# Optimization experiments

Hardware: AMD Instinct MI355X
Metric: run time of the kernel (lower is better)

Reference implementation:

```python
import jax, jax.numpy as jnp
import numpy as np

N_DST = [50000, 10000, 2048]
HEADS = 4


def setup_inputs() -> dict:
    key = jax.random.key(0)
    ks = jax.random.split(key, 32)
    d = {}
    d["x"] = jax.random.normal(ks[0], (200000, 128), jnp.float32)
    # conv fc weights [in, H*D], attn vectors [H, D], bias [H*D]; skip [in, out]+bias
    conv_dims = [(128, 64), (256, 64), (256, 47)]   # (in, per-head out D)
    skip_dims = [(128, 256), (256, 256), (256, 47)]
    for l, ((cin, dph), (sin, sout)) in enumerate(zip(conv_dims, skip_dims)):
        d[f"W{l}"] = 0.1 * jax.random.normal(ks[1 + 5 * l], (cin, HEADS * dph), jnp.float32)
        d[f"al{l}"] = 0.1 * jax.random.normal(ks[2 + 5 * l], (HEADS, dph), jnp.float32)
        d[f"ar{l}"] = 0.1 * jax.random.normal(ks[3 + 5 * l], (HEADS, dph), jnp.float32)
        d[f"b{l}"] = jnp.zeros((HEADS * dph,), jnp.float32)
        d[f"Ws{l}"] = 0.1 * jax.random.normal(ks[4 + 5 * l], (sin, sout), jnp.float32)
        d[f"bs{l}"] = jnp.zeros((sout,), jnp.float32)
    edge_cfg = [(800000, 200000, 50000), (400000, 50000, 10000), (100000, 10000, 2048)]
    for l, (ne, ns, nd) in enumerate(edge_cfg):
        d[f"src{l}"] = jax.random.randint(ks[20 + 2 * l], (ne,), 0, ns, jnp.int32)
        d[f"dst{l}"] = jax.random.randint(ks[21 + 2 * l], (ne,), 0, nd, jnp.int32)
    return d


def gat_conv(h_src, h_dst, src, dst, n_dst, W, al, ar, b):
    H, D = al.shape
    fs = (h_src @ W).reshape(-1, H, D)   # [n_src, H, D]
    fd = (h_dst @ W).reshape(-1, H, D)   # [n_dst, H, D]
    el = jnp.einsum("nhd,hd->nh", fs, al)
    er = jnp.einsum("nhd,hd->nh", fd, ar)
    e = jax.nn.leaky_relu(el[src] + er[dst], 0.2)          # [E, H]
    emax = jax.ops.segment_max(e, dst, num_segments=n_dst)  # stable softmax
    ee = jnp.exp(e - emax[dst])
    denom = jax.ops.segment_sum(ee, dst, num_segments=n_dst)
    alpha = ee / denom[dst]
    msg = fs[src] * alpha[:, :, None]                      # [E, H, D]
    rst = jax.ops.segment_sum(msg, dst, num_segments=n_dst)
    return rst + b.reshape(1, H, D)


def reference(x, W0, al0, ar0, b0, Ws0, bs0, W1, al1, ar1, b1, Ws1, bs1,
              W2, al2, ar2, b2, Ws2, bs2, src0, dst0, src1, dst1, src2, dst2):
    h = x
    # layer 0
    h_res = h[:N_DST[0]]
    h = gat_conv(h, h_res, src0, dst0, N_DST[0], W0, al0, ar0, b0).reshape(N_DST[0], -1)
    h = jax.nn.elu(h + h_res @ Ws0 + bs0)
    # layer 1
    h_res = h[:N_DST[1]]
    h = gat_conv(h, h_res, src1, dst1, N_DST[1], W1, al1, ar1, b1).reshape(N_DST[1], -1)
    h = jax.nn.elu(h + h_res @ Ws1 + bs1)
    # layer 2: mean over heads, no activation
    h_res = h[:N_DST[2]]
    h = gat_conv(h, h_res, src2, dst2, N_DST[2], W2, al2, ar2, b2).mean(axis=1)
    h = h + h_res @ Ws2 + bs2
    return jax.nn.log_softmax(h, axis=-1)
```

## Files before the change

### kernel.cpp

```cpp
#include <hip/hip_runtime.h>
#include <hip/hip_bf16.h>
#include <cmath>

#define HEADS 4
typedef __hip_bfloat16 bf16;
typedef short short8 __attribute__((ext_vector_type(8)));
typedef unsigned short us8 __attribute__((ext_vector_type(8)));
typedef float floatx4 __attribute__((ext_vector_type(4)));
typedef float floatx2 __attribute__((ext_vector_type(2)));
typedef unsigned int u32;

__device__ inline float bf2f(unsigned short u) {
    union { unsigned u; float f; } c; c.u = ((unsigned)u) << 16; return c.f;
}
__device__ inline short f2bs(float f) {
    bf16 h = __float2bfloat16(f);
    return *reinterpret_cast<short*>(&h);
}
__device__ __forceinline__ unsigned pack_bf16(float a, float b) {
    return (((unsigned)(unsigned short)f2bs(b)) << 16) | (unsigned short)f2bs(a);
}
__device__ __forceinline__ unsigned pack_fp8x4(float a, float b, float c, float d) {
    unsigned lo = __builtin_amdgcn_cvt_pk_fp8_f32(a, b, 0, false);
    return __builtin_amdgcn_cvt_pk_fp8_f32(c, d, lo, true);
}

__device__ __forceinline__ void ld_lds16(const void* g, void* l) {
    __builtin_amdgcn_global_load_lds((const __attribute__((address_space(1))) u32*)g,
                                     (__attribute__((address_space(3))) u32*)l, 16, 0, 0);
}

__device__ const int g_ND[3]   = {50000, 10000, 2048};
__device__ const int g_OOFF[3] = {0, 50001, 60002};
__device__ const int g_NE[3]   = {800000, 400000, 100000};
__device__ const int g_SOFF[3] = {0, 800000, 1200000};
__device__ const int g_S[3]    = {391, 79, 16};

#define NBIN 128
#define NBLK 128
#define MAXB 8192
#define MAXS 391
#define PF 4

__global__ void precast_all(const float* __restrict__ W0, const float* __restrict__ W1,
                            const float* __restrict__ W2, const float* __restrict__ W3,
                            const float* __restrict__ W4,
                            bf16* __restrict__ B0, bf16* __restrict__ B1, bf16* __restrict__ B2,
                            bf16* __restrict__ B3, bf16* __restrict__ B4)
{
    int y = blockIdx.y;
    const int Ks[5] = {128, 256, 256, 128, 256};
    const int Ns[5] = {256, 256, 188, 256, 256};
    const float* W = (y == 0) ? W0 : (y == 1) ? W1 : (y == 2) ? W2 : (y == 3) ? W3 : W4;
    bf16* B = (y == 0) ? B0 : (y == 1) ? B1 : (y == 2) ? B2 : (y == 3) ? B3 : B4;
    int K = Ks[y], N = Ns[y], sz = K * N;
    for (int i = blockIdx.x * blockDim.x + threadIdx.x; i < sz; i += gridDim.x * blockDim.x) {
        int n = i / K, k = i % K;
        B[i] = __float2bfloat16(W[(size_t)k * N + n]);
    }
}

template<int FUSE, int EL, int OUT8, int AF32>
__global__ __launch_bounds__(512)
void gemm_mfma(const void* __restrict__ Ain, const bf16* __restrict__ Bt,
               const bf16* __restrict__ add, const float* __restrict__ bias,
               const float* __restrict__ al, const float* __restrict__ ar,
               float* __restrict__ el, float* __restrict__ er,
               void* __restrict__ Cb, int M, int N, int K, int nd)
{
    const int BK = 64;
    __shared__ short As[128 * BK];
    __shared__ short Bs[256 * BK];
    int tid = threadIdx.x;
    int wave = tid >> 6, lane = tid & 63;
    int q = lane >> 4, r = lane & 15;
    int row0 = blockIdx.y * 128;
    int wm = (wave >> 2) * 64, wn = (wave & 3) * 64;

    const short* B16 = (const short*)Bt;
    int srow = tid >> 3;
    int scol = ((tid & 7) ^ (srow & 7)) * 8;
    const short* ga0; const short* ga1;
    const float* gaf0; const float* gaf1;
    if (AF32) {
        int arow0 = min(row0 + srow, M - 1);
        int arow1 = min(row0 + 64 + srow, M - 1);
        gaf0 = (const float*)Ain + (size_t)arow0 * K + scol;
        gaf1 = (const float*)Ain + (size_t)arow1 * K + scol;
        ga0 = ga1 = nullptr;
    } else {
        const short* A16 = (const short*)Ain;
        ga0 = A16 + (size_t)(row0 + srow) * K + scol;
        ga1 = ga0 + (size_t)64 * K;
        gaf0 = gaf1 = nullptr;
    }
    const short* gb = B16 + (size_t)srow * K + scol;
    char* la = (char*)As + tid * 16;
    char* lb = (char*)Bs + tid * 16;

    floatx4 zero = {0.f, 0.f, 0.f, 0.f};
    floatx4 acc[4][4];
#pragma unroll
    for (int i = 0; i < 4; i++)
#pragma unroll
        for (int j = 0; j < 4; j++) acc[i][j] = zero;

    for (int k0 = 0; k0 < K; k0 += BK) {
        ld_lds16(gb,                   lb);
        ld_lds16(gb + (size_t)64 * K,  lb + 8192);
        ld_lds16(gb + (size_t)128 * K, lb + 16384);
        ld_lds16(gb + (size_t)192 * K, lb + 24576);
        gb += BK;
        if (AF32) {
            float4 a0 = *(const float4*)gaf0;
            float4 a1 = *(const float4*)(gaf0 + 4);
            float4 b0 = *(const float4*)gaf1;
            float4 b1 = *(const float4*)(gaf1 + 4);
            uint4 w0 = {pack_bf16(a0.x, a0.y), pack_bf16(a0.z, a0.w),
                        pack_bf16(a1.x, a1.y), pack_bf16(a1.z, a1.w)};
            uint4 w1 = {pack_bf16(b0.x, b0.y), pack_bf16(b0.z, b0.w),
                        pack_bf16(b1.x, b1.y), pack_bf16(b1.z, b1.w)};
            *(uint4*)la = w0;
            *(uint4*)(la + 8192) = w1;
            gaf0 += BK; gaf1 += BK;
        } else {
            ld_lds16(ga0, la);
            ld_lds16(ga1, la + 8192);
            ga0 += BK; ga1 += BK;
        }
        __syncthreads();
#pragma unroll
        for (int ks = 0; ks < 2; ks++) {
            int gr = (((ks << 2) | q) ^ (r & 7)) * 8;
            short8 af[4], bfr[4];
#pragma unroll
            for (int mt = 0; mt < 4; mt++)
                af[mt] = *(short8*)&As[(wm + mt * 16 + r) * BK + gr];
#pragma unroll
            for (int nt = 0; nt < 4; nt++)
                bfr[nt] = *(short8*)&Bs[(wn + nt * 16 + r) * BK + gr];
#pragma unroll
            for (int mt = 0; mt < 4; mt++)
#pragma unroll
                for (int nt = 0; nt < 4; nt++)
                    acc[mt][nt] = __builtin_amdgcn_mfma_f32_16x16x32_bf16(bfr[nt], af[mt], acc[mt][nt], 0, 0, 0);
        }
        __syncthreads();
    }

#pragma unroll
    for (int mt = 0; mt < 4; mt++) {
        int grow = row0 + wm + mt * 16 + r;
        if (grow >= M) continue;
#pragma unroll
        for (int nt = 0; nt < 4; nt++) {
            int n0 = wn + nt * 16 + q * 4;
            floatx4 v = acc[mt][nt];
            if (FUSE == 1) {
                ushort4 ad = *(const ushort4*)&add[(size_t)grow * N + n0];
                float4 bi = *(const float4*)&bias[n0];
                v[0] += bf2f(ad.x) + bi.x;
                v[1] += bf2f(ad.y) + bi.y;
                v[2] += bf2f(ad.z) + bi.z;
                v[3] += bf2f(ad.w) + bi.w;
#pragma unroll
                for (int e = 0; e < 4; e++) v[e] = (v[e] > 0.f) ? v[e] : (__expf(v[e]) - 1.f);
            }
            if (OUT8) {
                *(u32*)((unsigned char*)Cb + (size_t)grow * N + n0) =
                    pack_fp8x4(v[0], v[1], v[2], v[3]);
            } else if (n0 + 3 < N) {
                uint2 o = {pack_bf16(v[0], v[1]), pack_bf16(v[2], v[3])};
                *(uint2*)((unsigned short*)Cb + (size_t)grow * N + n0) = o;
            } else {
#pragma unroll
                for (int e = 0; e < 4; e++)
                    if (n0 + e < N)
                        ((unsigned short*)Cb)[(size_t)grow * N + n0 + e] = (unsigned short)f2bs(v[e]);
            }
        }
    }

    if (EL) {
        int head = wave & 3;
#pragma unroll
        for (int mt = 0; mt < 4; mt++) {
            float pl = 0.f, pr = 0.f;
#pragma unroll
            for (int nt = 0; nt < 4; nt++) {
                int nn = nt * 16 + q * 4;
                float4 av = *(const float4*)&al[head * 64 + nn];
                float4 rv = *(const float4*)&ar[head * 64 + nn];
                floatx4 v = acc[mt][nt];
                pl += v[0] * av.x + v[1] * av.y + v[2] * av.z + v[3] * av.w;
                pr += v[0] * rv.x + v[1] * rv.y + v[2] * rv.z + v[3] * rv.w;
            }
            pl += __shfl_xor(pl, 16); pl += __shfl_xor(pl, 32);
            pr += __shfl_xor(pr, 16); pr += __shfl_xor(pr, 32);
            int grow = row0 + wm + mt * 16 + r;
            if (lane < 16 && grow < M) {
                el[grow * 4 + head] = pl;
                if (grow < nd) er[grow * 4 + head] = pr;
            }
        }
    }
}

__global__ void el_er_kernel(const bf16* __restrict__ fs, const float* __restrict__ al,
                             const float* __restrict__ ar, float* __restrict__ el,
                             float* __restrict__ er, int nd, int D)
{
    int n = blockIdx.x;
    int h = threadIdx.x >> 6;
    int d = threadIdx.x & 63;
    int HD = HEADS * D;
    float v = 0.f, a = 0.f, rr = 0.f;
    if (d < D) {
        v = __bfloat162float(fs[(size_t)n * HD + h * D + d]);
        a = al[h * D + d];
        rr = ar[h * D + d];
    }
    float pl = v * a, pr = v * rr;
    for (int off = 32; off; off >>= 1) {
        pl += __shfl_down(pl, off);
        pr += __shfl_down(pr, off);
    }
    if (d == 0) {
        el[n * HEADS + h] = pl;
        if (n < nd) er[n * HEADS + h] = pr;
    }
}

__global__ __launch_bounds__(256)
void bin_hist(const int* __restrict__ d0, const int* __restrict__ d1,
              const int* __restrict__ d2, int* __restrict__ blockhist)
{
    int l = blockIdx.y;
    const int* dst = (l == 0) ? d0 : (l == 1) ? d1 : d2;
    int ne = g_NE[l], S = g_S[l];
    __shared__ int h[NBIN];
    for (int i = threadIdx.x; i < NBIN; i += blockDim.x) h[i] = 0;
    __syncthreads();
    int per = (ne + NBLK - 1) / NBLK;
    int st = blockIdx.x * per;
    int en = min(st + per, ne);
    for (int i = st + threadIdx.x; i < en; i += blockDim.x)
        atomicAdd(&h[dst[i] / S], 1);
    __syncthreads();
    for (int i = threadIdx.x; i < NBIN; i += blockDim.x)
        blockhist[(l * NBIN + i) * NBLK + blockIdx.x] = h[i];
}

__global__ void coarse_scan(const int* __restrict__ blockhist, int* __restrict__ bbase,
                            int* __restrict__ offs)
{
    int l = blockIdx.x;
    int t = threadIdx.x;
    __shared__ int s[NBIN];
    int tot = 0;
    for (int k = 0; k < NBLK; k++) tot += blockhist[(l * NBIN + t) * NBLK + k];
    s[t] = tot;
    __syncthreads();
    for (int off = 1; off < NBIN; off <<= 1) {
        int a = (t >= off) ? s[t - off] : 0;
        __syncthreads();
        s[t] += a;
        __syncthreads();
    }
    bbase[l * (NBIN + 1) + t + 1] = s[t];
    if (t == 0) {
        bbase[l * (NBIN + 1)] = 0;
        offs[g_OOFF[l] + g_ND[l]] = g_NE[l];
    }
}

__global__ void bin_scan(const int* __restrict__ blockhist, const int* __restrict__ bbase,
                         int* __restrict__ base)
{
    int l = blockIdx.y, bin = blockIdx.x;
    int t = threadIdx.x;
    __shared__ int s[NBLK];
    int v = blockhist[(l * NBIN + bin) * NBLK + t];
    s[t] = v;
    __syncthreads();
    for (int off = 1; off < NBLK; off <<= 1) {
        int a = (t >= off) ? s[t - off] : 0;
        __syncthreads();
        s[t] += a;
        __syncthreads();
    }
    base[(l * NBIN + bin) * NBLK + t] = bbase[l * (NBIN + 1) + bin] + s[t] - v;
}

__global__ __launch_bounds__(256)
void bin_scatter(const int* __restrict__ s0, const int* __restrict__ d0,
                 const int* __restrict__ s1, const int* __restrict__ d1,
                 const int* __restrict__ s2, const int* __restrict__ d2,
                 const int* __restrict__ base, int* __restrict__ stage)
{
    int l = blockIdx.y;
    const int* src = (l == 0) ? s0 : (l == 1) ? s1 : s2;
    const int* dst = (l == 0) ? d0 : (l == 1) ? d1 : d2;
    int ne = g_NE[l], S = g_S[l], soff = g_SOFF[l];
    __shared__ int cur[NBIN];
    for (int i = threadIdx.x; i < NBIN; i += blockDim.x)
        cur[i] = base[(l * NBIN + i) * NBLK + blockIdx.x];
    __syncthreads();
    int per = (ne + NBLK - 1) / NBLK;
    int st = blockIdx.x * per;
    int en = min(st + per, ne);
    for (int i = st + threadIdx.x; i < en; i += blockDim.x) {
        int dv = dst[i];
        int b = dv / S;
        int ldst = dv - b * S;
        int p = atomicAdd(&cur[b], 1);
        stage[soff + p] = src[i] | (ldst << 18);
    }
}

__global__ __launch_bounds__(256)
void bin_expand(const int* __restrict__ stage, const int* __restrict__ bbase,
                int* __restrict__ offs, int* __restrict__ ssrc)
{
    int l = blockIdx.y, b = blockIdx.x;
    int S = g_S[l], nd = g_ND[l], ooff = g_OOFF[l], soff = g_SOFF[l];
    int dlo = b * S;
    if (dlo >= nd) return;
    int dhi = min(dlo + S, nd);
    int base = bbase[l * (NBIN + 1) + b];
    int end  = bbase[l * (NBIN + 1) + b + 1];
    int cnt  = end - base;
    int tid = threadIdx.x;
    __shared__ int sdata[MAXB];
    __shared__ int outb[MAXB];
    __shared__ int lh[512];
    __shared__ int lcur[MAXS];
    lh[tid] = 0; lh[tid + 256] = 0;
    __syncthreads();
    if (cnt <= MAXB) {
        for (int i = tid; i < cnt; i += 256) {
            int v = stage[soff + base + i];
            sdata[i] = v;
            atomicAdd(&lh[v >> 18], 1);
        }
        __syncthreads();
        for (int off = 1; off < 512; off <<= 1) {
            int a0 = (tid >= off) ? lh[tid - off] : 0;
            int a1 = lh[tid + 256 - off];
            __syncthreads();
            lh[tid] += a0; lh[tid + 256] += a1;
            __syncthreads();
        }
        for (int d = tid; d < dhi - dlo; d += 256) {
            int ex = (d == 0) ? 0 : lh[d - 1];
            offs[ooff + dlo + d] = base + ex;
            lcur[d] = ex;
        }
        __syncthreads();
        for (int i = tid; i < cnt; i += 256) {
            int v = sdata[i];
            int p = atomicAdd(&lcur[v >> 18], 1);
            outb[p] = v & 0x3FFFF;
        }
        __syncthreads();
        for (int i = tid; i < cnt; i += 256)
            ssrc[soff + base + i] = outb[i];
    } else {
        for (int i = tid; i < cnt; i += 256)
            atomicAdd(&lh[stage[soff + base + i] >> 18], 1);
        __syncthreads();
        for (int off = 1; off < 512; off <<= 1) {
            int a0 = (tid >= off) ? lh[tid - off] : 0;
            int a1 = lh[tid + 256 - off];
            __syncthreads();
            lh[tid] += a0; lh[tid + 256] += a1;
            __syncthreads();
        }
        for (int d = tid; d < dhi - dlo; d += 256) {
            int ex = (d == 0) ? 0 : lh[d - 1];
            offs[ooff + dlo + d] = base + ex;
            lcur[d] = ex;
        }
        __syncthreads();
        for (int i = tid; i < cnt; i += 256) {
            int v = stage[soff + base + i];
            int p = atomicAdd(&lcur[v >> 18], 1);
            ssrc[soff + base + p] = v & 0x3FFFF;
        }
    }
}

__global__ __launch_bounds__(256)
void attn_agg64(const unsigned char* __restrict__ fs8, const float* __restrict__ el,
                const float* __restrict__ er, const float* __restrict__ b,
                const int* __restrict__ offs, const int* __restrict__ ssrc,
                bf16* __restrict__ rst, int nd)
{
    int wave = threadIdx.x >> 6, lane = threadIdx.x & 63;
    int n = blockIdx.x * 4 + wave;
    if (n >= nd) return;
    int s0 = offs[n], s1 = offs[n + 1];
    float4 erv = *(const float4*)&er[(size_t)n * 4];
    int half = lane >> 5, sub = lane & 31, head = sub >> 3;
    float eh = (head == 0) ? erv.x : (head == 1) ? erv.y : (head == 2) ? erv.z : erv.w;

    floatx2 acc[4];
#pragma unroll
    for (int j = 0; j < 4; j++) acc[j] = (floatx2){0.f, 0.f};
    float s = 0.f;

    int cnt = s1 - s0;
    int npairs = cnt >> 1;
    int i = s0 + half;
    if (npairs > 0) {
        int sid = ssrc[i];
        float ev = el[(size_t)sid * 4 + head];
        uint2 f = *(const uint2*)&fs8[(size_t)sid * 256 + sub * 8];
        for (int p = 1; p < npairs; p++) {
            i += 2;
            int sid2 = ssrc[i];
            float ev2 = el[(size_t)sid2 * 4 + head];
            uint2 f2 = *(const uint2*)&fs8[(size_t)sid2 * 256 + sub * 8];
            float e = ev + eh; e = (e > 0.f) ? e : 0.2f * e;
            float a = __expf(fminf(e, 60.f));
            s += a;
            floatx2 aa = {a, a};
            acc[0] = __builtin_elementwise_fma((floatx2)__builtin_amdgcn_cvt_pk_f32_fp8(f.x, false), aa, acc[0]);
            acc[1] = __builtin_elementwise_fma((floatx2)__builtin_amdgcn_cvt_pk_f32_fp8(f.x, true),  aa, acc[1]);
            acc[2] = __builtin_elementwise_fma((floatx2)__builtin_amdgcn_cvt_pk_f32_fp8(f.y, false), aa, acc[2]);
            acc[3] = __builtin_elementwise_fma((floatx2)__builtin_amdgcn_cvt_pk_f32_fp8(f.y, true),  aa, acc[3]);
            ev = ev2; f = f2;
        }
        float e = ev + eh; e = (e > 0.f) ? e : 0.2f * e;
        float a = __expf(fminf(e, 60.f));
        s += a;
        floatx2 aa = {a, a};
        acc[0] = __builtin_elementwise_fma((floatx2)__builtin_amdgcn_cvt_pk_f32_fp8(f.x, false), aa, acc[0]);
        acc[1] = __builtin_elementwise_fma((floatx2)__builtin_amdgcn_cvt_pk_f32_fp8(f.x, true),  aa, acc[1]);
        acc[2] = __builtin_elementwise_fma((floatx2)__builtin_amdgcn_cvt_pk_f32_fp8(f.y, false), aa, acc[2]);
        acc[3] = __builtin_elementwise_fma((floatx2)__builtin_amdgcn_cvt_pk_f32_fp8(f.y, true),  aa, acc[3]);
    }
    if (cnt & 1) {
        int idx = s1 - 1;
        int sid = ssrc[idx];
        float ev = el[(size_t)sid * 4 + head];
        uint2 f = *(const uint2*)&fs8[(size_t)sid * 256 + sub * 8];
        float e = ev + eh; e = (e > 0.f) ? e : 0.2f * e;
        float a = __expf(fminf(e, 60.f));
        if (half) a = 0.f;
        s += a;
        floatx2 aa = {a, a};
        acc[0] = __builtin_elementwise_fma((floatx2)__builtin_amdgcn_cvt_pk_f32_fp8(f.x, false), aa, acc[0]);
        acc[1] = __builtin_elementwise_fma((floatx2)__builtin_amdgcn_cvt_pk_f32_fp8(f.x, true),  aa, acc[1]);
        acc[2] = __builtin_elementwise_fma((floatx2)__builtin_amdgcn_cvt_pk_f32_fp8(f.y, false), aa, acc[2]);
        acc[3] = __builtin_elementwise_fma((floatx2)__builtin_amdgcn_cvt_pk_f32_fp8(f.y, true),  aa, acc[3]);
    }
    s += __shfl_xor(s, 32);
#pragma unroll
    for (int j = 0; j < 4; j++) {
        acc[j].x += __shfl_xor(acc[j].x, 32);
        acc[j].y += __shfl_xor(acc[j].y, 32);
    }
    if (half == 0) {
        float inv = (s > 0.f) ? 1.f / s : 0.f;
        float4 b0 = *(const float4*)&b[sub * 8];
        float4 b1 = *(const float4*)&b[sub * 8 + 4];
        us8 o;
        o[0] = (unsigned short)f2bs(acc[0].x * inv + b0.x);
        o[1] = (unsigned short)f2bs(acc[0].y * inv + b0.y);
        o[2] = (unsigned short)f2bs(acc[1].x * inv + b0.z);
        o[3] = (unsigned short)f2bs(acc[1].y * inv + b0.w);
        o[4] = (unsigned short)f2bs(acc[2].x * inv + b1.x);
        o[5] = (unsigned short)f2bs(acc[2].y * inv + b1.y);
        o[6] = (unsigned short)f2bs(acc[3].x * inv + b1.z);
        o[7] = (unsigned short)f2bs(acc[3].y * inv + b1.w);
        *(us8*)&((unsigned short*)rst)[(size_t)n * 256 + sub * 8] = o;
    }
}

__global__ __launch_bounds__(256)
void attn_final_gen(const bf16* __restrict__ fs, const float* __restrict__ el,
                    const float* __restrict__ er, const float* __restrict__ b,
                    const int* __restrict__ offs, const int* __restrict__ ssrc,
                    const bf16* __restrict__ h2, const float* __restrict__ Ws,
                    const float* __restrict__ bs, float* __restrict__ out,
                    int D, int nd)
{
    __shared__ int slds[4][64];
    __shared__ __align__(16) float alds[4][64][4];
    __shared__ float flds[4][192];
    __shared__ unsigned short hlds[4][256];
    int wave = threadIdx.x >> 6, lane = threadIdx.x & 63;
    int n = blockIdx.x * 4 + wave;
    int HD = HEADS * D;
    int s0 = offs[n], s1 = offs[n + 1];
    int cnt = s1 - s0;
    float4 erv = *(const float4*)&er[(size_t)n * 4];
    const unsigned short* fsu = (const unsigned short*)fs;
    const unsigned short* h2u = (const unsigned short*)h2;

    *(ushort4*)&hlds[wave][lane * 4] = *(const ushort4*)&h2u[(size_t)n * 256 + lane * 4];

    bool act = (4 * lane) < HD;
    int h_[4];
#pragma unroll
    for (int j = 0; j < 4; j++) {
        int e = 4 * lane + j;
        h_[j] = (e < HD) ? (e / D) : 0;
    }
    float acc[4] = {0.f, 0.f, 0.f, 0.f};
    float sp0 = 0.f, sp1 = 0.f, sp2 = 0.f, sp3 = 0.f;

    for (int c0 = 0; c0 < cnt; c0 += 64) {
        int nc = min(cnt - c0, 64);
        if (lane < nc) {
            int sid = ssrc[s0 + c0 + lane];
            float4 ev = *(const float4*)&el[(size_t)sid * 4];
            float e0 = ev.x + erv.x; e0 = (e0 > 0.f) ? e0 : 0.2f * e0;
            float e1 = ev.y + erv.y; e1 = (e1 > 0.f) ? e1 : 0.2f * e1;
            float e2 = ev.z + erv.z; e2 = (e2 > 0.f) ? e2 : 0.2f * e2;
            float e3 = ev.w + erv.w; e3 = (e3 > 0.f) ? e3 : 0.2f * e3;
            float a0 = __expf(fminf(e0, 60.f));
            float a1 = __expf(fminf(e1, 60.f));
            float a2 = __expf(fminf(e2, 60.f));
            float a3 = __expf(fminf(e3, 60.f));
            sp0 += a0; sp1 += a1; sp2 += a2; sp3 += a3;
            slds[wave][lane] = sid;
            alds[wave][lane][0] = a0;
            alds[wave][lane][1] = a1;
            alds[wave][lane][2] = a2;
            alds[wave][lane][3] = a3;
        }
        __builtin_amdgcn_wave_barrier();
        float4 aq[PF]; ushort4 fq[PF];
#pragma unroll
        for (int k = 0; k < PF; k++) {
            if (k < nc) {
                int sid = slds[wave][k];
                aq[k] = *(const float4*)&alds[wave][k][0];
                fq[k] = act ? *(const ushort4*)&fsu[(size_t)sid * HD + 4 * lane]
                            : ushort4{0, 0, 0, 0};
            }
        }
        for (int eb = 0; eb < nc; eb += PF) {
#pragma unroll
            for (int k = 0; k < PF; k++) {
                int e = eb + k;
                if (e >= nc) break;
                float4 a4 = aq[k];
                ushort4 f = fq[k];
                int en = e + PF;
                if (en < nc) {
                    int sid = slds[wave][en];
                    aq[k] = *(const float4*)&alds[wave][en][0];
                    fq[k] = act ? *(const ushort4*)&fsu[(size_t)sid * HD + 4 * lane]
                                : ushort4{0, 0, 0, 0};
                }
                unsigned short fa[4] = {f.x, f.y, f.z, f.w};
#pragma unroll
                for (int j = 0; j < 4; j++) {
                    int hj = h_[j];
                    float av = (hj == 0) ? a4.x : (hj == 1) ? a4.y : (hj == 2) ? a4.z : a4.w;
                    acc[j] += av * bf2f(fa[j]);
                }
            }
        }
        __builtin_amdgcn_wave_barrier();
    }

#pragma unroll
    for (int off = 32; off; off >>= 1) {
        sp0 += __shfl_xor(sp0, off);
        sp1 += __shfl_xor(sp1, off);
        sp2 += __shfl_xor(sp2, off);
        sp3 += __shfl_xor(sp3, off);
    }
    if (act) {
#pragma unroll
        for (int j = 0; j < 4; j++) {
            int e4 = 4 * lane + j;
            int hj = h_[j];
            float sv = (hj == 0) ? sp0 : (hj == 1) ? sp1 : (hj == 2) ? sp2 : sp3;
            float o = (sv > 0.f) ? acc[j] / sv : 0.f;
            flds[wave][e4] = o + b[e4];
        }
    }
    __builtin_amdgcn_wave_barrier();

    const int C = 47;
    int c = lane;
    float v = -INFINITY;
    if (c < C) {
        float mean = 0.25f * (flds[wave][c] + flds[wave][C + c] +
                              flds[wave][2 * C + c] + flds[wave][3 * C + c]);
        float dot = 0.f;
#pragma unroll 4
        for (int k = 0; k < 256; k++)
            dot += bf2f(hlds[wave][k]) * Ws[k * C + c];
        v = mean + dot + bs[c];
    }
    float mx = v;
#pragma unroll
    for (int off = 32; off; off >>= 1) mx = fmaxf(mx, __shfl_xor(mx, off));
    float ex = (c < C) ? __expf(v - mx) : 0.f;
    float sum = ex;
#pragma unroll
    for (int off = 32; off; off >>= 1) sum += __shfl_xor(sum, off);
    if (c < C) out[n * C + c] = v - mx - logf(sum);
}

extern "C" void kernel_launch(void* const* d_in, const int* in_sizes, int n_in,
                              void* d_out, int out_size, void* d_ws, size_t ws_size,
                              hipStream_t stream)
{
    const float* x = (const float*)d_in[0];
    const float* W[3]  = {(const float*)d_in[1],  (const float*)d_in[7],  (const float*)d_in[13]};
    const float* al[3] = {(const float*)d_in[2],  (const float*)d_in[8],  (const float*)d_in[14]};
    const float* ar[3] = {(const float*)d_in[3],  (const float*)d_in[9],  (const float*)d_in[15]};
    const float* bb[3] = {(const float*)d_in[4],  (const float*)d_in[10], (const float*)d_in[16]};
    const float* Ws[3] = {(const float*)d_in[5],  (const float*)d_in[11], (const float*)d_in[17]};
    const float* bs[3] = {(const float*)d_in[6],  (const float*)d_in[12], (const float*)d_in[18]};
    const int* srcp[3] = {(const int*)d_in[19], (const int*)d_in[21], (const int*)d_in[23]};
    const int* dstp[3] = {(const int*)d_in[20], (const int*)d_in[22], (const int*)d_in[24]};

    char* p = (char*)d_ws;
    auto alloc = [&](size_t bytes) -> void* {
        void* r = (void*)p;
        p += (bytes + 255) & ~(size_t)255;
        return r;
    };
    bf16*  fsb   = (bf16*)alloc((size_t)200064 * 256 * 2);
    bf16*  h1b   = (bf16*)alloc((size_t)50048 * 256 * 2);
    bf16*  h2b   = (bf16*)alloc((size_t)10112 * 256 * 2);
    bf16*  rstb  = (bf16*)alloc((size_t)50000 * 256 * 2);
    float* elb   = (float*)alloc((size_t)200064 * 4 * 4);
    float* erb   = (float*)alloc((size_t)50048 * 4 * 4);
    bf16* Wt[3]; bf16* Wst[2];
    Wt[0]  = (bf16*)alloc(256 * 128 * 2);
    Wt[1]  = (bf16*)alloc(256 * 256 * 2);
    Wt[2]  = (bf16*)alloc(256 * 256 * 2);
    Wst[0] = (bf16*)alloc(256 * 128 * 2);
    Wst[1] = (bf16*)alloc(256 * 256 * 2);
    int* offs_all  = (int*)alloc(62051 * 4);
    int* ssrc_all  = (int*)alloc(1300000 * 4);
    int* stage_all = (int*)alloc(1300000 * 4);
    int* blockhist = (int*)alloc(3 * NBIN * NBLK * 4);
    int* binbase   = (int*)alloc(3 * NBIN * NBLK * 4);
    int* bbase     = (int*)alloc(3 * (NBIN + 1) * 4);

    unsigned char* fsb8 = (unsigned char*)fsb;

    const int OOFF[3] = {0, 50001, 60002};
    const int SOFF[3] = {0, 800000, 1200000};

    precast_all<<<dim3(128, 5), 256, 0, stream>>>(W[0], W[1], W[2], Ws[0], Ws[1],
                                                  Wt[0], Wt[1], Wt[2], Wst[0], Wst[1]);

    bin_hist<<<dim3(NBLK, 3), 256, 0, stream>>>(dstp[0], dstp[1], dstp[2], blockhist);
    coarse_scan<<<3, NBIN, 0, stream>>>(blockhist, bbase, offs_all);
    bin_scan<<<dim3(NBIN, 3), NBLK, 0, stream>>>(blockhist, bbase, binbase);
    bin_scatter<<<dim3(NBLK, 3), 256, 0, stream>>>(srcp[0], dstp[0], srcp[1], dstp[1],
                                                   srcp[2], dstp[2], binbase, stage_all);
    bin_expand<<<dim3(NBIN, 3), 256, 0, stream>>>(stage_all, bbase, offs_all, ssrc_all);

    gemm_mfma<0, 1, 1, 1><<<dim3(1, 1563), 512, 0, stream>>>(
        x, Wt[0], nullptr, nullptr, al[0], ar[0], elb, erb, fsb8, 200000, 256, 128, 50000);
    attn_agg64<<<12500, 256, 0, stream>>>(fsb8, elb, erb, bb[0], offs_all + OOFF[0], ssrc_all + SOFF[0], rstb, 50000);
    gemm_mfma<1, 0, 0, 1><<<dim3(1, 391), 512, 0, stream>>>(
        x, Wst[0], rstb, bs[0], nullptr, nullptr, nullptr, nullptr, h1b, 50000, 256, 128, 0);

    gemm_mfma<0, 1, 1, 0><<<dim3(1, 391), 512, 0, stream>>>(
        h1b, Wt[1], nullptr, nullptr, al[1], ar[1], elb, erb, fsb8, 50000, 256, 256, 10000);
    attn_agg64<<<2500, 256, 0, stream>>>(fsb8, elb, erb, bb[1], offs_all + OOFF[1], ssrc_all + SOFF[1], rstb, 10000);
    gemm_mfma<1, 0, 0, 0><<<dim3(1, 79), 512, 0, stream>>>(
        h1b, Wst[1], rstb, bs[1], nullptr, nullptr, nullptr, nullptr, h2b, 10000, 256, 256, 0);

    gemm_mfma<0, 0, 0, 0><<<dim3(1, 79), 512, 0, stream>>>(
        h2b, Wt[2], nullptr, nullptr, nullptr, nullptr, nullptr, nullptr, fsb, 10000, 188, 256, 0);
    el_er_kernel<<<10000, 256, 0, stream>>>(fsb, al[2], ar[2], elb, erb, 2048, 47);
    attn_final_gen<<<512, 256, 0, stream>>>(fsb, elb, erb, bb[2], offs_all + OOFF[2], ssrc_all + SOFF[2],
                                            h2b, Ws[2], bs[2], (float*)d_out, 47, 2048);
}
```

Baseline: 494.4 us.

## Fuse skip GEMM into conv GEMM and residual ELU into attention aggregation

The conv GEMM now also computes the skip projection h_res@Ws for destination rows, reusing the same A tile pointers and writing it to a bf16 buffer. The attention aggregation kernel then adds the skip result and bias and applies ELU before writing the next layer's input. This removes two separate skip GEMM launches and the round trip of the rst buffer. In exchange, the skip result is stored as bf16, and the first row blocks of each conv GEMM run a second K loop, so the work across blocks becomes uneven.

```diff
diff --git a/kernel.cpp b/kernel.cpp
--- a/kernel.cpp
+++ b/kernel.cpp
@@ -60,13 +60,14 @@
     }
 }
 
-template<int FUSE, int EL, int OUT8, int AF32>
+template<int FUSE, int EL, int OUT8, int AF32, int SKIP>
 __global__ __launch_bounds__(512)
 void gemm_mfma(const void* __restrict__ Ain, const bf16* __restrict__ Bt,
                const bf16* __restrict__ add, const float* __restrict__ bias,
                const float* __restrict__ al, const float* __restrict__ ar,
                float* __restrict__ el, float* __restrict__ er,
-               void* __restrict__ Cb, int M, int N, int K, int nd)
+               void* __restrict__ Cb, int M, int N, int K, int nd,
+               const bf16* __restrict__ Bt2, bf16* __restrict__ Cb2)
 {
     const int BK = 64;
     __shared__ short As[128 * BK];
@@ -80,21 +81,18 @@
     const short* B16 = (const short*)Bt;
     int srow = tid >> 3;
     int scol = ((tid & 7) ^ (srow & 7)) * 8;
-    const short* ga0; const short* ga1;
-    const float* gaf0; const float* gaf1;
+    const short* ga0s = nullptr; const short* ga1s = nullptr;
+    const float* gaf0s = nullptr; const float* gaf1s = nullptr;
     if (AF32) {
         int arow0 = min(row0 + srow, M - 1);
         int arow1 = min(row0 + 64 + srow, M - 1);
-        gaf0 = (const float*)Ain + (size_t)arow0 * K + scol;
-        gaf1 = (const float*)Ain + (size_t)arow1 * K + scol;
-        ga0 = ga1 = nullptr;
+        gaf0s = (const float*)Ain + (size_t)arow0 * K + scol;
+        gaf1s = (const float*)Ain + (size_t)arow1 * K + scol;
     } else {
         const short* A16 = (const short*)Ain;
-        ga0 = A16 + (size_t)(row0 + srow) * K + scol;
-        ga1 = ga0 + (size_t)64 * K;
-        gaf0 = gaf1 = nullptr;
-    }
-    const short* gb = B16 + (size_t)srow * K + scol;
+        ga0s = A16 + (size_t)(row0 + srow) * K + scol;
+        ga1s = ga0s + (size_t)64 * K;
+    }
     char* la = (char*)As + tid * 16;
     char* lb = (char*)Bs + tid * 16;
 
@@ -105,47 +103,52 @@
 #pragma unroll
         for (int j = 0; j < 4; j++) acc[i][j] = zero;
 
-    for (int k0 = 0; k0 < K; k0 += BK) {
-        ld_lds16(gb,                   lb);
-        ld_lds16(gb + (size_t)64 * K,  lb + 8192);
-        ld_lds16(gb + (size_t)128 * K, lb + 16384);
-        ld_lds16(gb + (size_t)192 * K, lb + 24576);
-        gb += BK;
-        if (AF32) {
-            float4 a0 = *(const float4*)gaf0;
-            float4 a1 = *(const float4*)(gaf0 + 4);
-            float4 b0 = *(const float4*)gaf1;
-            float4 b1 = *(const float4*)(gaf1 + 4);
-            uint4 w0 = {pack_bf16(a0.x, a0.y), pack_bf16(a0.z, a0.w),
-                        pack_bf16(a1.x, a1.y), pack_bf16(a1.z, a1.w)};
-            uint4 w1 = {pack_bf16(b0.x, b0.y), pack_bf16(b0.z, b0.w),
-                        pack_bf16(b1.x, b1.y), pack_bf16(b1.z, b1.w)};
-            *(uint4*)la = w0;
-            *(uint4*)(la + 8192) = w1;
-            gaf0 += BK; gaf1 += BK;
-        } else {
-            ld_lds16(ga0, la);
-            ld_lds16(ga1, la + 8192);
-            ga0 += BK; ga1 += BK;
-        }
-        __syncthreads();
-#pragma unroll
-        for (int ks = 0; ks < 2; ks++) {
-            int gr = (((ks << 2) | q) ^ (r & 7)) * 8;
-            short8 af[4], bfr[4];
-#pragma unroll
-            for (int mt = 0; mt < 4; mt++)
-                af[mt] = *(short8*)&As[(wm + mt * 16 + r) * BK + gr];
-#pragma unroll
-            for (int nt = 0; nt < 4; nt++)
-                bfr[nt] = *(short8*)&Bs[(wn + nt * 16 + r) * BK + gr];
-#pragma unroll
-            for (int mt = 0; mt < 4; mt++)
+    {
+        const short* gb = B16 + (size_t)srow * K + scol;
+        const short* ga0 = ga0s; const short* ga1 = ga1s;
+        const float* gaf0 = gaf0s; const float* gaf1 = gaf1s;
+        for (int k0 = 0; k0 < K; k0 += BK) {
+            ld_lds16(gb,                   lb);
+            ld_lds16(gb + (size_t)64 * K,  lb + 8192);
+            ld_lds16(gb + (size_t)128 * K, lb + 16384);
+            ld_lds16(gb + (size_t)192 * K, lb + 24576);
+            gb += BK;
+            if (AF32) {
+                float4 a0 = *(const float4*)gaf0;
+                float4 a1 = *(const float4*)(gaf0 + 4);
+                float4 b0 = *(const float4*)gaf1;
+                float4 b1 = *(const float4*)(gaf1 + 4);
+                uint4 w0 = {pack_bf16(a0.x, a0.y), pack_bf16(a0.z, a0.w),
+                            pack_bf16(a1.x, a1.y), pack_bf16(a1.z, a1.w)};
+                uint4 w1 = {pack_bf16(b0.x, b0.y), pack_bf16(b0.z, b0.w),
+                            pack_bf16(b1.x, b1.y), pack_bf16(b1.z, b1.w)};
+                *(uint4*)la = w0;
+                *(uint4*)(la + 8192) = w1;
+                gaf0 += BK; gaf1 += BK;
+            } else {
+                ld_lds16(ga0, la);
+                ld_lds16(ga1, la + 8192);
+                ga0 += BK; ga1 += BK;
+            }
+            __syncthreads();
+#pragma unroll
+            for (int ks = 0; ks < 2; ks++) {
+                int gr = (((ks << 2) | q) ^ (r & 7)) * 8;
+                short8 af[4], bfr[4];
+#pragma unroll
+                for (int mt = 0; mt < 4; mt++)
+                    af[mt] = *(short8*)&As[(wm + mt * 16 + r) * BK + gr];
 #pragma unroll
                 for (int nt = 0; nt < 4; nt++)
-                    acc[mt][nt] = __builtin_amdgcn_mfma_f32_16x16x32_bf16(bfr[nt], af[mt], acc[mt][nt], 0, 0, 0);
-        }
-        __syncthreads();
+                    bfr[nt] = *(short8*)&Bs[(wn + nt * 16 + r) * BK + gr];
+#pragma unroll
+                for (int mt = 0; mt < 4; mt++)
+#pragma unroll
+                    for (int nt = 0; nt < 4; nt++)
+                        acc[mt][nt] = __builtin_amdgcn_mfma_f32_16x16x32_bf16(bfr[nt], af[mt], acc[mt][nt], 0, 0, 0);
+            }
+            __syncthreads();
+        }
     }
 
 #pragma unroll
@@ -201,6 +204,71 @@
             if (lane < 16 && grow < M) {
                 el[grow * 4 + head] = pl;
                 if (grow < nd) er[grow * 4 + head] = pr;
+            }
+        }
+    }
+
+    if (SKIP) {
+        if (row0 >= nd) return;
+#pragma unroll
+        for (int i = 0; i < 4; i++)
+#pragma unroll
+            for (int j = 0; j < 4; j++) acc[i][j] = zero;
+        const short* gb2 = (const short*)Bt2 + (size_t)srow * K + scol;
+        const short* ga0 = ga0s; const short* ga1 = ga1s;
+        const float* gaf0 = gaf0s; const float* gaf1 = gaf1s;
+        for (int k0 = 0; k0 < K; k0 += BK) {
+            ld_lds16(gb2,                   lb);
+            ld_lds16(gb2 + (size_t)64 * K,  lb + 8192);
+            ld_lds16(gb2 + (size_t)128 * K, lb + 16384);
+            ld_lds16(gb2 + (size_t)192 * K, lb + 24576);
+            gb2 += BK;
+            if (AF32) {
+                float4 a0 = *(const float4*)gaf0;
+                float4 a1 = *(const float4*)(gaf0 + 4);
+                float4 b0 = *(const float4*)gaf1;
+                float4 b1 = *(const float4*)(gaf1 + 4);
+                uint4 w0 = {pack_bf16(a0.x, a0.y), pack_bf16(a0.z, a0.w),
+                            pack_bf16(a1.x, a1.y), pack_bf16(a1.z, a1.w)};
+                uint4 w1 = {pack_bf16(b0.x, b0.y), pack_bf16(b0.z, b0.w),
+                            pack_bf16(b1.x, b1.y), pack_bf16(b1.z, b1.w)};
+                *(uint4*)la = w0;
+                *(uint4*)(la + 8192) = w1;
+                gaf0 += BK; gaf1 += BK;
+            } else {
+                ld_lds16(ga0, la);
+                ld_lds16(ga1, la + 8192);
+                ga0 += BK; ga1 += BK;
+            }
+            __syncthreads();
+#pragma unroll
+            for (int ks = 0; ks < 2; ks++) {
+                int gr = (((ks << 2) | q) ^ (r & 7)) * 8;
+                short8 af[4], bfr[4];
+#pragma unroll
+                for (int mt = 0; mt < 4; mt++)
+                    af[mt] = *(short8*)&As[(wm + mt * 16 + r) * BK + gr];
+#pragma unroll
+                for (int nt = 0; nt < 4; nt++)
+                    bfr[nt] = *(short8*)&Bs[(wn + nt * 16 + r) * BK + gr];
+#pragma unroll
+                for (int mt = 0; mt < 4; mt++)
+#pragma unroll
+                    for (int nt = 0; nt < 4; nt++)
+                        acc[mt][nt] = __builtin_amdgcn_mfma_f32_16x16x32_bf16(bfr[nt], af[mt], acc[mt][nt], 0, 0, 0);
+            }
+            __syncthreads();
+        }
+#pragma unroll
+        for (int mt = 0; mt < 4; mt++) {
+            int grow = row0 + wm + mt * 16 + r;
+            if (grow >= nd) continue;
+#pragma unroll
+            for (int nt = 0; nt < 4; nt++) {
+                int n0 = wn + nt * 16 + q * 4;
+                floatx4 v = acc[mt][nt];
+                uint2 o = {pack_bf16(v[0], v[1]), pack_bf16(v[2], v[3])};
+                *(uint2*)((unsigned short*)Cb2 + (size_t)grow * 256 + n0) = o;
             }
         }
     }
@@ -390,10 +458,12 @@
     }
 }
 
+template<int FUSEH>
 __global__ __launch_bounds__(256)
 void attn_agg64(const unsigned char* __restrict__ fs8, const float* __restrict__ el,
                 const float* __restrict__ er, const float* __restrict__ b,
                 const int* __restrict__ offs, const int* __restrict__ ssrc,
+                const bf16* __restrict__ xs, const float* __restrict__ bs2,
                 bf16* __restrict__ rst, int nd)
 {
     int wave = threadIdx.x >> 6, lane = threadIdx.x & 63;
@@ -465,15 +535,29 @@
         float inv = (s > 0.f) ? 1.f / s : 0.f;
         float4 b0 = *(const float4*)&b[sub * 8];
         float4 b1 = *(const float4*)&b[sub * 8 + 4];
+        float vals[8];
+        vals[0] = acc[0].x * inv + b0.x;
+        vals[1] = acc[0].y * inv + b0.y;
+        vals[2] = acc[1].x * inv + b0.z;
+        vals[3] = acc[1].y * inv + b0.w;
+        vals[4] = acc[2].x * inv + b1.x;
+        vals[5] = acc[2].y * inv + b1.y;
+        vals[6] = acc[3].x * inv + b1.z;
+        vals[7] = acc[3].y * inv + b1.w;
+        if (FUSEH) {
+            us8 xv = *(const us8*)&((const unsigned short*)xs)[(size_t)n * 256 + sub * 8];
+            float4 s0v = *(const float4*)&bs2[sub * 8];
+            float4 s1v = *(const float4*)&bs2[sub * 8 + 4];
+            float sb[8] = {s0v.x, s0v.y, s0v.z, s0v.w, s1v.x, s1v.y, s1v.z, s1v.w};
+#pragma unroll
+            for (int j = 0; j < 8; j++) {
+                float v = vals[j] + bf2f(xv[j]) + sb[j];
+                vals[j] = (v > 0.f) ? v : (__expf(v) - 1.f);
+            }
+        }
         us8 o;
-        o[0] = (unsigned short)f2bs(acc[0].x * inv + b0.x);
-        o[1] = (unsigned short)f2bs(acc[0].y * inv + b0.y);
-        o[2] = (unsigned short)f2bs(acc[1].x * inv + b0.z);
-        o[3] = (unsigned short)f2bs(acc[1].y * inv + b0.w);
-        o[4] = (unsigned short)f2bs(acc[2].x * inv + b1.x);
-        o[5] = (unsigned short)f2bs(acc[2].y * inv + b1.y);
-        o[6] = (unsigned short)f2bs(acc[3].x * inv + b1.z);
-        o[7] = (unsigned short)f2bs(acc[3].y * inv + b1.w);
+#pragma unroll
+        for (int j = 0; j < 8; j++) o[j] = (unsigned short)f2bs(vals[j]);
         *(us8*)&((unsigned short*)rst)[(size_t)n * 256 + sub * 8] = o;
     }
 }
@@ -632,7 +716,7 @@
     bf16*  fsb   = (bf16*)alloc((size_t)200064 * 256 * 2);
     bf16*  h1b   = (bf16*)alloc((size_t)50048 * 256 * 2);
     bf16*  h2b   = (bf16*)alloc((size_t)10112 * 256 * 2);
-    bf16*  rstb  = (bf16*)alloc((size_t)50000 * 256 * 2);
+    bf16*  xsb   = (bf16*)alloc((size_t)50048 * 256 * 2);
     float* elb   = (float*)alloc((size_t)200064 * 4 * 4);
     float* erb   = (float*)alloc((size_t)50048 * 4 * 4);
     bf16* Wt[3]; bf16* Wst[2];
@@ -663,20 +747,21 @@
                                                    srcp[2], dstp[2], binbase, stage_all);
     bin_expand<<<dim3(NBIN, 3), 256, 0, stream>>>(stage_all, bbase, offs_all, ssrc_all);
 
-    gemm_mfma<0, 1, 1, 1><<<dim3(1, 1563), 512, 0, stream>>>(
-        x, Wt[0], nullptr, nullptr, al[0], ar[0], elb, erb, fsb8, 200000, 256, 128, 50000);
-    attn_agg64<<<12500, 256, 0, stream>>>(fsb8, elb, erb, bb[0], offs_all + OOFF[0], ssrc_all + SOFF[0], rstb, 50000);
-    gemm_mfma<1, 0, 0, 1><<<dim3(1, 391), 512, 0, stream>>>(
-        x, Wst[0], rstb, bs[0], nullptr, nullptr, nullptr, nullptr, h1b, 50000, 256, 128, 0);
-
-    gemm_mfma<0, 1, 1, 0><<<dim3(1, 391), 512, 0, stream>>>(
-        h1b, Wt[1], nullptr, nullptr, al[1], ar[1], elb, erb, fsb8, 50000, 256, 256, 10000);
-    attn_agg64<<<2500, 256, 0, stream>>>(fsb8, elb, erb, bb[1], offs_all + OOFF[1], ssrc_all + SOFF[1], rstb, 10000);
-    gemm_mfma<1, 0, 0, 0><<<dim3(1, 79), 512, 0, stream>>>(
-        h1b, Wst[1], rstb, bs[1], nullptr, nullptr, nullptr, nullptr, h2b, 10000, 256, 256, 0);
-
-    gemm_mfma<0, 0, 0, 0><<<dim3(1, 79), 512, 0, stream>>>(
-        h2b, Wt[2], nullptr, nullptr, nullptr, nullptr, nullptr, nullptr, fsb, 10000, 188, 256, 0);
+    gemm_mfma<0, 1, 1, 1, 1><<<dim3(1, 1563), 512, 0, stream>>>(
+        x, Wt[0], nullptr, nullptr, al[0], ar[0], elb, erb, fsb8, 200000, 256, 128, 50000,
+        Wst[0], xsb);
+    attn_agg64<1><<<12500, 256, 0, stream>>>(fsb8, elb, erb, bb[0], offs_all + OOFF[0],
+                                             ssrc_all + SOFF[0], xsb, bs[0], h1b, 50000);
+
+    gemm_mfma<0, 1, 1, 0, 1><<<dim3(1, 391), 512, 0, stream>>>(
+        h1b, Wt[1], nullptr, nullptr, al[1], ar[1], elb, erb, fsb8, 50000, 256, 256, 10000,
+        Wst[1], xsb);
+    attn_agg64<1><<<2500, 256, 0, stream>>>(fsb8, elb, erb, bb[1], offs_all + OOFF[1],
+                                            ssrc_all + SOFF[1], xsb, bs[1], h2b, 10000);
+
+    gemm_mfma<0, 0, 0, 0, 0><<<dim3(1, 79), 512, 0, stream>>>(
+        h2b, Wt[2], nullptr, nullptr, nullptr, nullptr, nullptr, nullptr, fsb, 10000, 188, 256, 0,
+        nullptr, nullptr);
     el_er_kernel<<<10000, 256, 0, stream>>>(fsb, al[2], ar[2], elb, erb, 2048, 47);
     attn_final_gen<<<512, 256, 0, stream>>>(fsb, elb, erb, bb[2], offs_all + OOFF[2], ssrc_all + SOFF[2],
                                             h2b, Ws[2], bs[2], (float*)d_out, 47, 2048);
```

New measurement: 470.1 us. -4.9%, faster.
